# Performance work log

Measured on AMD Instinct MI355X. Metric: run time of the kernel, lower is better.

## Reference

```python
import jax, jax.numpy as jnp
import numpy as np

N_NODES = 163840
N_EDGES = 2621440
F_IN = 64
F_HID = 64
SUBG = 20  # size_subgraph_samples
NEG_SLOPE = 0.2


def gat_conv(x, src, dst, W, a_src, a_dst, b):
    """PyG GATConv, heads=1, concat. src/dst already include self-loops."""
    n = x.shape[0]
    h = x @ W                               # [N, H]
    al_s = h @ a_src                        # [N]
    al_d = h @ a_dst                        # [N]
    e = jax.nn.leaky_relu(al_s[src] + al_d[dst], NEG_SLOPE)  # [E]
    # softmax over incoming edges of each dst node
    m = jax.ops.segment_max(e, dst, num_segments=n)
    ex = jnp.exp(e - m[dst])
    denom = jax.ops.segment_sum(ex, dst, num_segments=n)
    alpha = ex / (denom[dst] + 1e-16)
    msg = h[src] * alpha[:, None]           # [E, H]
    out = jax.ops.segment_sum(msg, dst, num_segments=n)
    return out + b


def setup_inputs() -> dict:
    key = jax.random.key(0)
    ks = jax.random.split(key, 12)
    s = 0.05
    return {
        "x": jax.random.normal(ks[0], (N_NODES, F_IN), jnp.float32),
        "edge_index": jax.random.randint(ks[1], (2, N_EDGES), 0, N_NODES, jnp.int64 if jax.config.jax_enable_x64 else jnp.int32),
        "W1": jax.random.normal(ks[2], (F_IN, F_HID), jnp.float32) * s,
        "a_src1": jax.random.normal(ks[3], (F_HID,), jnp.float32) * s,
        "a_dst1": jax.random.normal(ks[4], (F_HID,), jnp.float32) * s,
        "b1": jnp.zeros((F_HID,), jnp.float32),
        "W2": jax.random.normal(ks[5], (F_HID, F_HID), jnp.float32) * s,
        "a_src2": jax.random.normal(ks[6], (F_HID,), jnp.float32) * s,
        "a_dst2": jax.random.normal(ks[7], (F_HID,), jnp.float32) * s,
        "b2": jnp.zeros((F_HID,), jnp.float32),
        "W_out": jax.random.normal(ks[8], (F_HID * SUBG, 1), jnp.float32) * s,
        "b_out": jnp.zeros((1,), jnp.float32),
    }


def reference(x, edge_index, W1, a_src1, a_dst1, b1, W2, a_src2, a_dst2, b2, W_out, b_out):
    n = x.shape[0]
    loop = jnp.arange(n, dtype=edge_index.dtype)
    src = jnp.concatenate([edge_index[0], loop])  # add_self_loops=True
    dst = jnp.concatenate([edge_index[1], loop])
    h = gat_conv(x, src, dst, W1, a_src1, a_dst1, b1)
    h = jax.nn.relu(h)  # dropout is identity in eval mode
    h = gat_conv(h, src, dst, W2, a_src2, a_dst2, b2)
    h = jax.nn.relu(h)
    h = h.reshape(n // SUBG, F_HID * SUBG)
    return h @ W_out + b_out
```

## Files before the change

kernel.cpp:

```cpp
#include <hip/hip_runtime.h>
#include <math.h>

#define F 64
#define NPB 160
#define BCAP 3584

typedef __attribute__((ext_vector_type(8))) short bf16x8;
typedef __attribute__((ext_vector_type(4))) float f32x4;

__device__ inline unsigned short f2bf(float f) {
  unsigned int u = __float_as_uint(f);
  u += 0x7fffu + ((u >> 16) & 1u);
  return (unsigned short)(u >> 16);
}

__global__ __launch_bounds__(256) void k_prep(const float* __restrict__ W1, const float* __restrict__ W2,
                                              uint4* __restrict__ wf, int* __restrict__ bcnt, int nb,
                                              float* __restrict__ out, const float* __restrict__ bo, int ng,
                                              int* __restrict__ ssrc, int e) {
  int tid = threadIdx.x;
  if (blockIdx.x == 0) {
    for (int i = tid; i < 1024; i += 256) {
      int layer = i >> 9, rem = i & 511;
      int cb = rem >> 6, lane = rem & 63;
      int c = cb >> 1, kk = cb & 1;
      int l15 = lane & 15, quad = lane >> 4;
      const float* W = layer ? W2 : W1;
      unsigned short p[8];
      #pragma unroll
      for (int j = 0; j < 8; j++) {
        int kd = kk * 32 + quad * 8 + j;
        p[j] = f2bf(W[kd * F + c * 16 + l15]);
      }
      wf[i] = *(const uint4*)p;
    }
  } else {
    for (int i = tid; i < nb * 16; i += 256) bcnt[i] = 0;
    float b0 = bo[0];
    for (int i = tid; i < ng; i += 256) out[i] = b0;
    if (tid < 64) ssrc[e + tid] = 0;
  }
}

__device__ __forceinline__ void gemm_body(const float* __restrict__ in, const uint4* __restrict__ wf,
                                          const float* __restrict__ avs, const float* __restrict__ avd,
                                          unsigned short* __restrict__ hgb, float* __restrict__ als,
                                          float* __restrict__ ald, int n, int bid, int nbl) {
  int tid = threadIdx.x, lane = tid & 63, wv = tid >> 6;
  int l15 = lane & 15, quad = lane >> 4;
  bf16x8 bfr[4][2];
  #pragma unroll
  for (int cb = 0; cb < 8; cb++) {
    uint4 u = wf[cb * 64 + lane];
    bfr[cb >> 1][cb & 1] = *(const bf16x8*)&u;
  }
  float as_l[4], ad_l[4];
  #pragma unroll
  for (int c = 0; c < 4; c++) { as_l[c] = avs[c * 16 + l15]; ad_l[c] = avd[c * 16 + l15]; }

  int nchunks = n >> 6;
  for (int chunk = bid; chunk < nchunks; chunk += nbl) {
    int r0 = (chunk << 6) + (wv << 4);
    bf16x8 a0, a1;
    const float4* xr = (const float4*)(in + (size_t)(r0 + l15) * F + quad * 8);
    float4 xa = xr[0], xb = xr[1];
    float4 xc = xr[8], xd = xr[9];
    a0[0] = (short)f2bf(xa.x); a0[1] = (short)f2bf(xa.y); a0[2] = (short)f2bf(xa.z); a0[3] = (short)f2bf(xa.w);
    a0[4] = (short)f2bf(xb.x); a0[5] = (short)f2bf(xb.y); a0[6] = (short)f2bf(xb.z); a0[7] = (short)f2bf(xb.w);
    a1[0] = (short)f2bf(xc.x); a1[1] = (short)f2bf(xc.y); a1[2] = (short)f2bf(xc.z); a1[3] = (short)f2bf(xc.w);
    a1[4] = (short)f2bf(xd.x); a1[5] = (short)f2bf(xd.y); a1[6] = (short)f2bf(xd.z); a1[7] = (short)f2bf(xd.w);
    f32x4 cfr[4];
    #pragma unroll
    for (int c = 0; c < 4; c++) {
      cfr[c] = (f32x4){0.f, 0.f, 0.f, 0.f};
      cfr[c] = __builtin_amdgcn_mfma_f32_16x16x32_bf16(a0, bfr[c][0], cfr[c], 0, 0, 0);
      cfr[c] = __builtin_amdgcn_mfma_f32_16x16x32_bf16(a1, bfr[c][1], cfr[c], 0, 0, 0);
    }
    #pragma unroll
    for (int i = 0; i < 4; i++) {
      int row = r0 + quad * 4 + i;
      #pragma unroll
      for (int c = 0; c < 4; c++) hgb[(size_t)row * F + c * 16 + l15] = f2bf(cfr[c][i]);
      float ps = cfr[0][i] * as_l[0] + cfr[1][i] * as_l[1] + cfr[2][i] * as_l[2] + cfr[3][i] * as_l[3];
      float pd = cfr[0][i] * ad_l[0] + cfr[1][i] * ad_l[1] + cfr[2][i] * ad_l[2] + cfr[3][i] * ad_l[3];
      #pragma unroll
      for (int o = 1; o <= 8; o <<= 1) { ps += __shfl_xor(ps, o); pd += __shfl_xor(pd, o); }
      if (l15 == 0) { als[row] = ps; ald[row] = pd; }
    }
  }
}

__global__ __launch_bounds__(256) void k_scatter_gemm1(const int* __restrict__ esrc, const int* __restrict__ edst,
                                                       int* __restrict__ bcnt, unsigned int* __restrict__ binned,
                                                       int e, int ch, int S,
                                                       const float* __restrict__ x, const uint4* __restrict__ wf,
                                                       const float* __restrict__ avs, const float* __restrict__ avd,
                                                       unsigned short* __restrict__ hgb, float* __restrict__ als,
                                                       float* __restrict__ ald, int n) {
  int k = blockIdx.x, tid = threadIdx.x;
  if (k < S) {
    __shared__ int hist[1024];
    __shared__ int cur[1024];
    for (int i = tid; i < 1024; i += 256) hist[i] = 0;
    __syncthreads();
    int beg = k * ch, end = min(e, beg + ch);
    int len = end - beg;
    if (len <= 0) return;
    int nv = len >> 2;
    for (int g = tid; g < nv; g += 256) {
      int4 d4 = *(const int4*)(edst + beg + (g << 2));
      atomicAdd(&hist[d4.x / NPB], 1);
      atomicAdd(&hist[d4.y / NPB], 1);
      atomicAdd(&hist[d4.z / NPB], 1);
      atomicAdd(&hist[d4.w / NPB], 1);
    }
    for (int i = beg + (nv << 2) + tid; i < end; i += 256) atomicAdd(&hist[edst[i] / NPB], 1);
    __syncthreads();
    for (int b = tid; b < 1024; b += 256) {
      int c = hist[b];
      int base = 0;
      if (c) base = atomicAdd(&bcnt[b * 16], c);
      cur[b] = b * BCAP + base;
    }
    __syncthreads();
    for (int g = tid; g < nv; g += 256) {
      int i = beg + (g << 2);
      int4 d4 = *(const int4*)(edst + i);
      int4 s4 = *(const int4*)(esrc + i);
      #pragma unroll
      for (int j = 0; j < 4; j++) {
        int d = (j == 0) ? d4.x : (j == 1) ? d4.y : (j == 2) ? d4.z : d4.w;
        int s = (j == 0) ? s4.x : (j == 1) ? s4.y : (j == 2) ? s4.z : s4.w;
        int b = d / NPB;
        int p = atomicAdd(&cur[b], 1);
        if (p < (b + 1) * BCAP) binned[p] = (unsigned int)s | ((unsigned int)(d - b * NPB) << 24);
      }
    }
    for (int i = beg + (nv << 2) + tid; i < end; i += 256) {
      int d = edst[i];
      int b = d / NPB;
      int p = atomicAdd(&cur[b], 1);
      if (p < (b + 1) * BCAP) binned[p] = (unsigned int)esrc[i] | ((unsigned int)(d - b * NPB) << 24);
    }
    return;
  }
  gemm_body(x, wf, avs, avd, hgb, als, ald, n, k - S, (int)gridDim.x - S);
}

__global__ __launch_bounds__(256) void k_bucket_csr(const unsigned int* __restrict__ binned,
                                                    const int* __restrict__ bcnt,
                                                    int* __restrict__ ssrc, int* __restrict__ offs,
                                                    int n, int nb) {
  __shared__ int ncnt[NPB];
  __shared__ int cur[NPB];
  __shared__ int red[256];
  __shared__ int wsum[4];
  __shared__ int stage[BCAP];
  int b = blockIdx.x, tid = threadIdx.x;
  int lane = tid & 63, wv = tid >> 6;
  int acc = 0;
  for (int j = tid; j < b; j += 256) acc += min(bcnt[j * 16], BCAP);
  red[tid] = acc;
  __syncthreads();
  #pragma unroll
  for (int o = 128; o > 0; o >>= 1) {
    if (tid < o) red[tid] += red[tid + o];
    __syncthreads();
  }
  int outbase = red[0];
  int ecnt = min(bcnt[b * 16], BCAP);
  int node0 = b * NPB;
  int nn = min(NPB, n - node0);
  const uint4* bq = (const uint4*)(binned + (size_t)b * BCAP);
  int nv4 = ecnt >> 2;
  for (int i = tid; i < NPB; i += 256) ncnt[i] = 0;
  __syncthreads();
  for (int i = tid; i < nv4; i += 256) {
    uint4 q = bq[i];
    atomicAdd(&ncnt[q.x >> 24], 1);
    atomicAdd(&ncnt[q.y >> 24], 1);
    atomicAdd(&ncnt[q.z >> 24], 1);
    atomicAdd(&ncnt[q.w >> 24], 1);
  }
  for (int i = (nv4 << 2) + tid; i < ecnt; i += 256)
    atomicAdd(&ncnt[binned[(size_t)b * BCAP + i] >> 24], 1);
  __syncthreads();
  int v = (tid < nn) ? ncnt[tid] : 0;
  int x = v;
  #pragma unroll
  for (int o = 1; o <= 32; o <<= 1) { int y = __shfl_up(x, o); if (lane >= o) x += y; }
  if (lane == 63) wsum[wv] = x;
  __syncthreads();
  int add = 0;
  for (int w = 0; w < wv; w++) add += wsum[w];
  int incl = x + add;
  if (tid < nn) {
    int noff = incl - v;
    cur[tid] = noff;
    offs[node0 + tid] = outbase + noff;
  }
  __syncthreads();
  for (int i = tid; i < nv4; i += 256) {
    uint4 q = bq[i];
    int p0 = atomicAdd(&cur[q.x >> 24], 1); stage[p0] = (int)(q.x & 0xFFFFFFu);
    int p1 = atomicAdd(&cur[q.y >> 24], 1); stage[p1] = (int)(q.y & 0xFFFFFFu);
    int p2 = atomicAdd(&cur[q.z >> 24], 1); stage[p2] = (int)(q.z & 0xFFFFFFu);
    int p3 = atomicAdd(&cur[q.w >> 24], 1); stage[p3] = (int)(q.w & 0xFFFFFFu);
  }
  for (int i = (nv4 << 2) + tid; i < ecnt; i += 256) {
    unsigned int q = binned[(size_t)b * BCAP + i];
    int p = atomicAdd(&cur[q >> 24], 1);
    stage[p] = (int)(q & 0xFFFFFFu);
  }
  __syncthreads();
  for (int i = tid; i < ecnt; i += 256) ssrc[outbase + i] = stage[i];
  if (b == nb - 1 && tid == 0) offs[n] = outbase + ecnt;
}

__device__ __forceinline__ void agg_node(int node, int n, const int* __restrict__ offs,
                                         const int* __restrict__ ssrc,
                                         const uint4* __restrict__ hg4,
                                         const float* __restrict__ als,
                                         const float* __restrict__ ald,
                                         float4 bl0, float4 bl1, int l8, float r[8]) {
  int cnode = min(node, n - 1);
  int beg = offs[cnode];
  int deg = offs[cnode + 1] - beg;
  float aldv = ald[cnode];

  float ts = als[cnode] + aldv;
  ts = fmaxf(ts, 0.2f * ts);
  float exs = __expf(ts);
  float s = exs;
  uint4 us = hg4[(size_t)cnode * 8 + l8];
  float acc[8];
  acc[0] = exs * __uint_as_float(us.x << 16);
  acc[1] = exs * __uint_as_float(us.x & 0xffff0000u);
  acc[2] = exs * __uint_as_float(us.y << 16);
  acc[3] = exs * __uint_as_float(us.y & 0xffff0000u);
  acc[4] = exs * __uint_as_float(us.z << 16);
  acc[5] = exs * __uint_as_float(us.z & 0xffff0000u);
  acc[6] = exs * __uint_as_float(us.w << 16);
  acc[7] = exs * __uint_as_float(us.w & 0xffff0000u);

  #pragma unroll 4
  for (int j = 0; j < deg; j++) {
    int src = ssrc[beg + j];
    float t = als[src] + aldv;
    t = fmaxf(t, 0.2f * t);
    float ex = __expf(t);
    s += ex;
    uint4 u = hg4[(size_t)src * 8 + l8];
    acc[0] = fmaf(ex, __uint_as_float(u.x << 16), acc[0]);
    acc[1] = fmaf(ex, __uint_as_float(u.x & 0xffff0000u), acc[1]);
    acc[2] = fmaf(ex, __uint_as_float(u.y << 16), acc[2]);
    acc[3] = fmaf(ex, __uint_as_float(u.y & 0xffff0000u), acc[3]);
    acc[4] = fmaf(ex, __uint_as_float(u.z << 16), acc[4]);
    acc[5] = fmaf(ex, __uint_as_float(u.z & 0xffff0000u), acc[5]);
    acc[6] = fmaf(ex, __uint_as_float(u.w << 16), acc[6]);
    acc[7] = fmaf(ex, __uint_as_float(u.w & 0xffff0000u), acc[7]);
  }

  float iv = 1.f / (s + 1e-16f);
  r[0] = fmaxf(fmaf(acc[0], iv, bl0.x), 0.f);
  r[1] = fmaxf(fmaf(acc[1], iv, bl0.y), 0.f);
  r[2] = fmaxf(fmaf(acc[2], iv, bl0.z), 0.f);
  r[3] = fmaxf(fmaf(acc[3], iv, bl0.w), 0.f);
  r[4] = fmaxf(fmaf(acc[4], iv, bl1.x), 0.f);
  r[5] = fmaxf(fmaf(acc[5], iv, bl1.y), 0.f);
  r[6] = fmaxf(fmaf(acc[6], iv, bl1.z), 0.f);
  r[7] = fmaxf(fmaf(acc[7], iv, bl1.w), 0.f);
}

__global__ __launch_bounds__(256) void k_spmm_g2(const int* __restrict__ offs, const int* __restrict__ ssrc,
                                                 const unsigned short* __restrict__ hgb,
                                                 const float* __restrict__ als, const float* __restrict__ ald,
                                                 const float* __restrict__ bias, const uint4* __restrict__ wf2,
                                                 const float* __restrict__ avs, const float* __restrict__ avd,
                                                 unsigned short* __restrict__ hgb2, float* __restrict__ als2,
                                                 float* __restrict__ ald2, int n) {
  __shared__ __align__(16) unsigned short hsh[64][72];
  int tid = threadIdx.x, lane = tid & 63, wv = tid >> 6;
  int g8 = lane >> 3, l8 = lane & 7;
  const uint4* hg4 = (const uint4*)hgb;
  float4 bl0 = ((const float4*)bias)[l8 * 2];
  float4 bl1 = ((const float4*)bias)[l8 * 2 + 1];

  for (int p = 0; p < 2; p++) {
    int row = p * 32 + wv * 8 + g8;
    int node = blockIdx.x * 64 + row;
    float r[8];
    agg_node(node, n, offs, ssrc, hg4, als, ald, bl0, bl1, l8, r);
    unsigned short pk[8];
    #pragma unroll
    for (int k = 0; k < 8; k++) pk[k] = f2bf(r[k]);
    *(uint4*)&hsh[row][l8 * 8] = *(const uint4*)pk;
  }
  __syncthreads();

  int l15 = lane & 15, quad = lane >> 4;
  bf16x8 bfr[4][2];
  #pragma unroll
  for (int cb = 0; cb < 8; cb++) {
    uint4 u = wf2[cb * 64 + lane];
    bfr[cb >> 1][cb & 1] = *(const bf16x8*)&u;
  }
  float as_l[4], ad_l[4];
  #pragma unroll
  for (int c = 0; c < 4; c++) { as_l[c] = avs[c * 16 + l15]; ad_l[c] = avd[c * 16 + l15]; }

  int r0 = wv << 4;
  uint4 u0 = *(const uint4*)&hsh[r0 + l15][quad * 8];
  uint4 u1 = *(const uint4*)&hsh[r0 + l15][quad * 8 + 32];
  bf16x8 a0 = *(const bf16x8*)&u0;
  bf16x8 a1 = *(const bf16x8*)&u1;
  f32x4 cfr[4];
  #pragma unroll
  for (int c = 0; c < 4; c++) {
    cfr[c] = (f32x4){0.f, 0.f, 0.f, 0.f};
    cfr[c] = __builtin_amdgcn_mfma_f32_16x16x32_bf16(a0, bfr[c][0], cfr[c], 0, 0, 0);
    cfr[c] = __builtin_amdgcn_mfma_f32_16x16x32_bf16(a1, bfr[c][1], cfr[c], 0, 0, 0);
  }
  #pragma unroll
  for (int i = 0; i < 4; i++) {
    int row = blockIdx.x * 64 + r0 + quad * 4 + i;
    #pragma unroll
    for (int c = 0; c < 4; c++) hgb2[(size_t)row * F + c * 16 + l15] = f2bf(cfr[c][i]);
    float ps = cfr[0][i] * as_l[0] + cfr[1][i] * as_l[1] + cfr[2][i] * as_l[2] + cfr[3][i] * as_l[3];
    float pd = cfr[0][i] * ad_l[0] + cfr[1][i] * ad_l[1] + cfr[2][i] * ad_l[2] + cfr[3][i] * ad_l[3];
    #pragma unroll
    for (int o = 1; o <= 8; o <<= 1) { ps += __shfl_xor(ps, o); pd += __shfl_xor(pd, o); }
    if (l15 == 0) { als2[row] = ps; ald2[row] = pd; }
  }
}

__global__ __launch_bounds__(256) void k_spmm_out(const int* __restrict__ offs, const int* __restrict__ ssrc,
                                                  const unsigned short* __restrict__ hgb,
                                                  const float* __restrict__ als, const float* __restrict__ ald,
                                                  const float* __restrict__ bias, const float* __restrict__ Wout,
                                                  float* __restrict__ out, int n) {
  int tid = threadIdx.x, lane = tid & 63, wv = tid >> 6;
  int g8 = lane >> 3, l8 = lane & 7;
  const uint4* hg4 = (const uint4*)hgb;
  float4 bl0 = ((const float4*)bias)[l8 * 2];
  float4 bl1 = ((const float4*)bias)[l8 * 2 + 1];

  __shared__ float gsl[3];
  if (tid < 3) gsl[tid] = 0.f;

  int node = (blockIdx.x * 4 + wv) * 8 + g8;
  bool nodeok = node < n;
  int cnode = min(node, n - 1);
  float r[8];
  agg_node(node, n, offs, ssrc, hg4, als, ald, bl0, bl1, l8, r);

  int node0 = blockIdx.x * 32;
  int grp0 = node0 / 20;
  int grp = cnode / 20, slot = cnode - grp * 20;
  const float* wr = Wout + slot * F + l8 * 8;
  float dot = 0.f;
  #pragma unroll
  for (int k = 0; k < 8; k++) dot = fmaf(r[k], wr[k], dot);
  #pragma unroll
  for (int o = 1; o <= 4; o <<= 1) dot += __shfl_xor(dot, o);
  __syncthreads();
  if (nodeok && l8 == 0) atomicAdd(&gsl[grp - grp0], dot);
  __syncthreads();
  if (tid < 3) {
    float v = gsl[tid];
    if (v != 0.f) atomicAdd(out + grp0 + tid, v);
  }
}

extern "C" void kernel_launch(void* const* d_in, const int* in_sizes, int n_in,
                              void* d_out, int out_size, void* d_ws, size_t ws_size,
                              hipStream_t stream) {
  const float* x   = (const float*)d_in[0];
  const int*   ei  = (const int*)d_in[1];
  const float* W1  = (const float*)d_in[2];
  const float* as1 = (const float*)d_in[3];
  const float* ad1 = (const float*)d_in[4];
  const float* b1  = (const float*)d_in[5];
  const float* W2  = (const float*)d_in[6];
  const float* as2 = (const float*)d_in[7];
  const float* ad2 = (const float*)d_in[8];
  const float* b2  = (const float*)d_in[9];
  const float* Wo  = (const float*)d_in[10];
  const float* bo  = (const float*)d_in[11];
  float* out = (float*)d_out;

  const int N = in_sizes[0] / F;
  const int E = in_sizes[1] / 2;
  const int* esrc = ei;
  const int* edst = ei + E;

  size_t off = 0;
  auto alloc = [&](size_t bytes) -> void* {
    void* p = (char*)d_ws + off;
    off += (bytes + 255) & ~(size_t)255;
    return p;
  };
  unsigned short* hgb  = (unsigned short*)alloc((size_t)N * F * 2);
  unsigned short* hgb2 = (unsigned short*)alloc((size_t)N * F * 2);
  float* als  = (float*)alloc((size_t)N * 4);
  float* ald  = (float*)alloc((size_t)N * 4);
  float* als2 = (float*)alloc((size_t)N * 4);
  float* ald2 = (float*)alloc((size_t)N * 4);
  int* offs   = (int*)alloc((size_t)(N + 1) * 4);
  int* bcnt   = (int*)alloc((size_t)1024 * 16 * 4);
  int* ssrc   = (int*)alloc((size_t)(E + 64) * 4);
  unsigned int* binned = (unsigned int*)alloc((size_t)1024 * BCAP * 4);
  uint4* wf   = (uint4*)alloc(16384);
  (void)ws_size; (void)n_in; (void)out_size;

  const int NG = N / 20;
  const int NB = (N + NPB - 1) / NPB;
  const int S = 256;
  const int CH = (((E + S - 1) / S) + 3) & ~3;

  k_prep<<<2, 256, 0, stream>>>(W1, W2, wf, bcnt, NB, out, bo, NG, ssrc, E);
  k_scatter_gemm1<<<S + (N >> 6), 256, 0, stream>>>(esrc, edst, bcnt, binned, E, CH, S,
                                                    x, wf, as1, ad1, hgb, als, ald, N);
  k_bucket_csr<<<NB, 256, 0, stream>>>(binned, bcnt, ssrc, offs, N, NB);
  k_spmm_g2<<<(N >> 6), 256, 0, stream>>>(offs, ssrc, hgb, als, ald, b1, wf + 512, as2, ad2,
                                          hgb2, als2, ald2, N);
  k_spmm_out<<<(N >> 5), 256, 0, stream>>>(offs, ssrc, hgb2, als2, ald2, b2, Wo, out, N);
}
```

Measured before the change: 274.9 us.

## Fuse CSR bucket build with layer-1 aggregation and layer-2 GEMM

Merges the bucket-to-CSR kernel with the first-layer attention aggregation and second-layer MFMA projection. Each block aggregates its 160 nodes straight from the shared-memory staged source list, so the ssrc/offs round trip through global memory and one launch are avoided. The cost is much larger LDS use per block (stage plus a 160x72 bf16 tile), which lowers occupancy. Parallelism also drops to 1024 blocks of 4 waves doing 5 passes each, which may hurt latency hiding for the gather-heavy aggregation.

New measurement: 270.5 us. No clear change (-1.6%).

```diff
diff --git a/kernel.cpp b/kernel.cpp
--- a/kernel.cpp
+++ b/kernel.cpp
@@ -16,8 +16,7 @@
 
 __global__ __launch_bounds__(256) void k_prep(const float* __restrict__ W1, const float* __restrict__ W2,
                                               uint4* __restrict__ wf, int* __restrict__ bcnt, int nb,
-                                              float* __restrict__ out, const float* __restrict__ bo, int ng,
-                                              int* __restrict__ ssrc, int e) {
+                                              float* __restrict__ out, const float* __restrict__ bo, int ng) {
   int tid = threadIdx.x;
   if (blockIdx.x == 0) {
     for (int i = tid; i < 1024; i += 256) {
@@ -38,7 +37,6 @@
     for (int i = tid; i < nb * 16; i += 256) bcnt[i] = 0;
     float b0 = bo[0];
     for (int i = tid; i < ng; i += 256) out[i] = b0;
-    if (tid < 64) ssrc[e + tid] = 0;
   }
 }
 
@@ -147,17 +145,25 @@
   gemm_body(x, wf, avs, avd, hgb, als, ald, n, k - S, (int)gridDim.x - S);
 }
 
-__global__ __launch_bounds__(256) void k_bucket_csr(const unsigned int* __restrict__ binned,
-                                                    const int* __restrict__ bcnt,
-                                                    int* __restrict__ ssrc, int* __restrict__ offs,
-                                                    int n, int nb) {
+__global__ __launch_bounds__(256) void k_csr_g2(const unsigned int* __restrict__ binned,
+                                                const int* __restrict__ bcnt,
+                                                int* __restrict__ ssrc, int* __restrict__ offs,
+                                                const unsigned short* __restrict__ hgb,
+                                                const float* __restrict__ als, const float* __restrict__ ald,
+                                                const float* __restrict__ bias, const uint4* __restrict__ wf2,
+                                                const float* __restrict__ avs, const float* __restrict__ avd,
+                                                unsigned short* __restrict__ hgb2, float* __restrict__ als2,
+                                                float* __restrict__ ald2, int n, int nb) {
   __shared__ int ncnt[NPB];
+  __shared__ int noff[NPB];
   __shared__ int cur[NPB];
-  __shared__ int red[256];
   __shared__ int wsum[4];
   __shared__ int stage[BCAP];
+  __shared__ __align__(16) unsigned short hsh[NPB][72];
   int b = blockIdx.x, tid = threadIdx.x;
   int lane = tid & 63, wv = tid >> 6;
+  int* red = stage;
+
   int acc = 0;
   for (int j = tid; j < b; j += 256) acc += min(bcnt[j * 16], BCAP);
   red[tid] = acc;
@@ -195,9 +201,10 @@
   for (int w = 0; w < wv; w++) add += wsum[w];
   int incl = x + add;
   if (tid < nn) {
-    int noff = incl - v;
-    cur[tid] = noff;
-    offs[node0 + tid] = outbase + noff;
+    int nf = incl - v;
+    noff[tid] = nf;
+    cur[tid] = nf;
+    offs[node0 + tid] = outbase + nf;
   }
   __syncthreads();
   for (int i = tid; i < nv4; i += 256) {
@@ -215,6 +222,113 @@
   __syncthreads();
   for (int i = tid; i < ecnt; i += 256) ssrc[outbase + i] = stage[i];
   if (b == nb - 1 && tid == 0) offs[n] = outbase + ecnt;
+
+  int g8 = lane >> 3, l8 = lane & 7;
+  const uint4* hg4 = (const uint4*)hgb;
+  float4 bl0 = ((const float4*)bias)[l8 * 2];
+  float4 bl1 = ((const float4*)bias)[l8 * 2 + 1];
+
+  for (int p = 0; p < 5; p++) {
+    int row = p * 32 + wv * 8 + g8;
+    int node = node0 + row;
+    bool rowok = row < nn;
+    int cnode = min(node, n - 1);
+    int deg = rowok ? ncnt[row] : 0;
+    int lbeg = rowok ? noff[row] : 0;
+    float aldv = ald[cnode];
+
+    float ts = als[cnode] + aldv;
+    ts = fmaxf(ts, 0.2f * ts);
+    float exs = __expf(ts);
+    float s = exs;
+    uint4 us = hg4[(size_t)cnode * 8 + l8];
+    float acc8[8];
+    acc8[0] = exs * __uint_as_float(us.x << 16);
+    acc8[1] = exs * __uint_as_float(us.x & 0xffff0000u);
+    acc8[2] = exs * __uint_as_float(us.y << 16);
+    acc8[3] = exs * __uint_as_float(us.y & 0xffff0000u);
+    acc8[4] = exs * __uint_as_float(us.z << 16);
+    acc8[5] = exs * __uint_as_float(us.z & 0xffff0000u);
+    acc8[6] = exs * __uint_as_float(us.w << 16);
+    acc8[7] = exs * __uint_as_float(us.w & 0xffff0000u);
+
+    #pragma unroll 4
+    for (int j = 0; j < deg; j++) {
+      int src = stage[lbeg + j];
+      float t = als[src] + aldv;
+      t = fmaxf(t, 0.2f * t);
+      float ex = __expf(t);
+      s += ex;
+      uint4 u = hg4[(size_t)src * 8 + l8];
+      acc8[0] = fmaf(ex, __uint_as_float(u.x << 16), acc8[0]);
+      acc8[1] = fmaf(ex, __uint_as_float(u.x & 0xffff0000u), acc8[1]);
+      acc8[2] = fmaf(ex, __uint_as_float(u.y << 16), acc8[2]);
+      acc8[3] = fmaf(ex, __uint_as_float(u.y & 0xffff0000u), acc8[3]);
+      acc8[4] = fmaf(ex, __uint_as_float(u.z << 16), acc8[4]);
+      acc8[5] = fmaf(ex, __uint_as_float(u.z & 0xffff0000u), acc8[5]);
+      acc8[6] = fmaf(ex, __uint_as_float(u.w << 16), acc8[6]);
+      acc8[7] = fmaf(ex, __uint_as_float(u.w & 0xffff0000u), acc8[7]);
+    }
+
+    float iv = 1.f / (s + 1e-16f);
+    float r[8];
+    r[0] = fmaxf(fmaf(acc8[0], iv, bl0.x), 0.f);
+    r[1] = fmaxf(fmaf(acc8[1], iv, bl0.y), 0.f);
+    r[2] = fmaxf(fmaf(acc8[2], iv, bl0.z), 0.f);
+    r[3] = fmaxf(fmaf(acc8[3], iv, bl0.w), 0.f);
+    r[4] = fmaxf(fmaf(acc8[4], iv, bl1.x), 0.f);
+    r[5] = fmaxf(fmaf(acc8[5], iv, bl1.y), 0.f);
+    r[6] = fmaxf(fmaf(acc8[6], iv, bl1.z), 0.f);
+    r[7] = fmaxf(fmaf(acc8[7], iv, bl1.w), 0.f);
+    unsigned short pk[8];
+    #pragma unroll
+    for (int kk = 0; kk < 8; kk++) pk[kk] = f2bf(r[kk]);
+    *(uint4*)&hsh[row][l8 * 8] = *(const uint4*)pk;
+  }
+  __syncthreads();
+
+  int l15 = lane & 15, quad = lane >> 4;
+  bf16x8 bfr[4][2];
+  #pragma unroll
+  for (int cb = 0; cb < 8; cb++) {
+    uint4 u = wf2[cb * 64 + lane];
+    bfr[cb >> 1][cb & 1] = *(const bf16x8*)&u;
+  }
+  float as_l[4], ad_l[4];
+  #pragma unroll
+  for (int c = 0; c < 4; c++) { as_l[c] = avs[c * 16 + l15]; ad_l[c] = avd[c * 16 + l15]; }
+
+  #pragma unroll
+  for (int t = 0; t < 3; t++) {
+    int strip = t * 4 + wv;
+    if (strip < 10) {
+      int r0 = strip << 4;
+      uint4 u0 = *(const uint4*)&hsh[r0 + l15][quad * 8];
+      uint4 u1 = *(const uint4*)&hsh[r0 + l15][quad * 8 + 32];
+      bf16x8 a0 = *(const bf16x8*)&u0;
+      bf16x8 a1 = *(const bf16x8*)&u1;
+      f32x4 cfr[4];
+      #pragma unroll
+      for (int c = 0; c < 4; c++) {
+        cfr[c] = (f32x4){0.f, 0.f, 0.f, 0.f};
+        cfr[c] = __builtin_amdgcn_mfma_f32_16x16x32_bf16(a0, bfr[c][0], cfr[c], 0, 0, 0);
+        cfr[c] = __builtin_amdgcn_mfma_f32_16x16x32_bf16(a1, bfr[c][1], cfr[c], 0, 0, 0);
+      }
+      #pragma unroll
+      for (int i = 0; i < 4; i++) {
+        int row = node0 + r0 + quad * 4 + i;
+        if (row < n) {
+          #pragma unroll
+          for (int c = 0; c < 4; c++) hgb2[(size_t)row * F + c * 16 + l15] = f2bf(cfr[c][i]);
+        }
+        float ps = cfr[0][i] * as_l[0] + cfr[1][i] * as_l[1] + cfr[2][i] * as_l[2] + cfr[3][i] * as_l[3];
+        float pd = cfr[0][i] * ad_l[0] + cfr[1][i] * ad_l[1] + cfr[2][i] * ad_l[2] + cfr[3][i] * ad_l[3];
+        #pragma unroll
+        for (int o = 1; o <= 8; o <<= 1) { ps += __shfl_xor(ps, o); pd += __shfl_xor(pd, o); }
+        if (l15 == 0 && row < n) { als2[row] = ps; ald2[row] = pd; }
+      }
+    }
+  }
 }
 
 __device__ __forceinline__ void agg_node(int node, int n, const int* __restrict__ offs,
@@ -270,68 +384,6 @@
   r[5] = fmaxf(fmaf(acc[5], iv, bl1.y), 0.f);
   r[6] = fmaxf(fmaf(acc[6], iv, bl1.z), 0.f);
   r[7] = fmaxf(fmaf(acc[7], iv, bl1.w), 0.f);
-}
-
-__global__ __launch_bounds__(256) void k_spmm_g2(const int* __restrict__ offs, const int* __restrict__ ssrc,
-                                                 const unsigned short* __restrict__ hgb,
-                                                 const float* __restrict__ als, const float* __restrict__ ald,
-                                                 const float* __restrict__ bias, const uint4* __restrict__ wf2,
-                                                 const float* __restrict__ avs, const float* __restrict__ avd,
-                                                 unsigned short* __restrict__ hgb2, float* __restrict__ als2,
-                                                 float* __restrict__ ald2, int n) {
-  __shared__ __align__(16) unsigned short hsh[64][72];
-  int tid = threadIdx.x, lane = tid & 63, wv = tid >> 6;
-  int g8 = lane >> 3, l8 = lane & 7;
-  const uint4* hg4 = (const uint4*)hgb;
-  float4 bl0 = ((const float4*)bias)[l8 * 2];
-  float4 bl1 = ((const float4*)bias)[l8 * 2 + 1];
-
-  for (int p = 0; p < 2; p++) {
-    int row = p * 32 + wv * 8 + g8;
-    int node = blockIdx.x * 64 + row;
-    float r[8];
-    agg_node(node, n, offs, ssrc, hg4, als, ald, bl0, bl1, l8, r);
-    unsigned short pk[8];
-    #pragma unroll
-    for (int k = 0; k < 8; k++) pk[k] = f2bf(r[k]);
-    *(uint4*)&hsh[row][l8 * 8] = *(const uint4*)pk;
-  }
-  __syncthreads();
-
-  int l15 = lane & 15, quad = lane >> 4;
-  bf16x8 bfr[4][2];
-  #pragma unroll
-  for (int cb = 0; cb < 8; cb++) {
-    uint4 u = wf2[cb * 64 + lane];
-    bfr[cb >> 1][cb & 1] = *(const bf16x8*)&u;
-  }
-  float as_l[4], ad_l[4];
-  #pragma unroll
-  for (int c = 0; c < 4; c++) { as_l[c] = avs[c * 16 + l15]; ad_l[c] = avd[c * 16 + l15]; }
-
-  int r0 = wv << 4;
-  uint4 u0 = *(const uint4*)&hsh[r0 + l15][quad * 8];
-  uint4 u1 = *(const uint4*)&hsh[r0 + l15][quad * 8 + 32];
-  bf16x8 a0 = *(const bf16x8*)&u0;
-  bf16x8 a1 = *(const bf16x8*)&u1;
-  f32x4 cfr[4];
-  #pragma unroll
-  for (int c = 0; c < 4; c++) {
-    cfr[c] = (f32x4){0.f, 0.f, 0.f, 0.f};
-    cfr[c] = __builtin_amdgcn_mfma_f32_16x16x32_bf16(a0, bfr[c][0], cfr[c], 0, 0, 0);
-    cfr[c] = __builtin_amdgcn_mfma_f32_16x16x32_bf16(a1, bfr[c][1], cfr[c], 0, 0, 0);
-  }
-  #pragma unroll
-  for (int i = 0; i < 4; i++) {
-    int row = blockIdx.x * 64 + r0 + quad * 4 + i;
-    #pragma unroll
-    for (int c = 0; c < 4; c++) hgb2[(size_t)row * F + c * 16 + l15] = f2bf(cfr[c][i]);
-    float ps = cfr[0][i] * as_l[0] + cfr[1][i] * as_l[1] + cfr[2][i] * as_l[2] + cfr[3][i] * as_l[3];
-    float pd = cfr[0][i] * ad_l[0] + cfr[1][i] * ad_l[1] + cfr[2][i] * ad_l[2] + cfr[3][i] * ad_l[3];
-    #pragma unroll
-    for (int o = 1; o <= 8; o <<= 1) { ps += __shfl_xor(ps, o); pd += __shfl_xor(pd, o); }
-    if (l15 == 0) { als2[row] = ps; ald2[row] = pd; }
-  }
 }
 
 __global__ __launch_bounds__(256) void k_spmm_out(const int* __restrict__ offs, const int* __restrict__ ssrc,
@@ -418,11 +470,10 @@
   const int S = 256;
   const int CH = (((E + S - 1) / S) + 3) & ~3;
 
-  k_prep<<<2, 256, 0, stream>>>(W1, W2, wf, bcnt, NB, out, bo, NG, ssrc, E);
+  k_prep<<<2, 256, 0, stream>>>(W1, W2, wf, bcnt, NB, out, bo, NG);
   k_scatter_gemm1<<<S + (N >> 6), 256, 0, stream>>>(esrc, edst, bcnt, binned, E, CH, S,
                                                     x, wf, as1, ad1, hgb, als, ald, N);
-  k_bucket_csr<<<NB, 256, 0, stream>>>(binned, bcnt, ssrc, offs, N, NB);
-  k_spmm_g2<<<(N >> 6), 256, 0, stream>>>(offs, ssrc, hgb, als, ald, b1, wf + 512, as2, ad2,
-                                          hgb2, als2, ald2, N);
+  k_csr_g2<<<NB, 256, 0, stream>>>(binned, bcnt, ssrc, offs, hgb, als, ald, b1,
+                                   wf + 512, as2, ad2, hgb2, als2, ald2, N, NB);
   k_spmm_out<<<(N >> 5), 256, 0, stream>>>(offs, ssrc, hgb2, als2, ald2, b2, Wo, out, N);
 }
```
